# Performance work log

Measured on AMD Instinct MI355X. Metric: run time of the kernel, lower is better.

Reference implementation:

```python
import jax, jax.numpy as jnp
import numpy as np

H, W = 256, 256
N = 1024          # gaussians
G = 2             # num_gabor
RANK = 6          # abundance channels / endmembers
C = 128           # spectral bands
LORA_ALPHA = 0.1


def setup_inputs() -> dict:
    key = jax.random.key(0)
    ks = jax.random.split(key, 8)
    xyz = 0.5 * jax.random.normal(ks[0], (N, 2), jnp.float32)          # pre-tanh means
    cholesky = jnp.zeros((N, 3), jnp.float32)                           # + bound -> identity-ish cov
    feat0 = jnp.log(jnp.expm1(jnp.float32(0.05)))                       # inverse softplus(0.05)
    features_dc = feat0 + 0.01 * jax.random.normal(ks[1], (N, RANK), jnp.float32)
    gabor_freqs = (jax.random.uniform(ks[2], (N * G, 2), jnp.float32) - 0.5) * 0.002
    gabor_weights = jax.random.uniform(ks[3], (N * G, 1), jnp.float32) * -5.0
    lora_U = 0.3 * jax.random.normal(ks[4], (RANK, 2), jnp.float32)
    lora_V = 0.001 * jax.random.normal(ks[5], (2, C), jnp.float32)
    lora_scale_logit = jnp.zeros((1,), jnp.float32)
    opacity = jnp.ones((N, 1), jnp.float32)
    endmember = jax.random.uniform(ks[6], (RANK, C), jnp.float32)
    return {"xyz": xyz, "cholesky": cholesky, "features_dc": features_dc,
            "gabor_freqs": gabor_freqs, "gabor_weights": gabor_weights,
            "lora_U": lora_U, "lora_V": lora_V, "lora_scale_logit": lora_scale_logit,
            "opacity": opacity, "endmember": endmember}


def _rasterize_gabor_sum(xyz, cholesky, features_dc, gabor_freqs, gabor_weights, opacity):
    # project_gaussians_2d: tanh means in [-1,1] -> pixel coords
    means = jnp.tanh(xyz)                                               # [N,2]
    centers = (means * 0.5 + 0.5) * jnp.array([W, H], jnp.float32)      # [N,2] (x,y)
    ch = cholesky + jnp.array([0.5, 0.0, 0.5], jnp.float32)             # cholesky bound
    l1, l2, l3 = ch[:, 0], ch[:, 1], ch[:, 2]
    # Sigma = L L^T, L = [[l1,0],[l2,l3]] -> conic = Sigma^{-1}
    a = l1 * l1
    b = l1 * l2
    c = l2 * l2 + l3 * l3
    det = a * c - b * b
    ca, cb, cc = c / det, -b / det, a / det                             # [N]
    # pixel grid, row-major flat index p = y*W + x, pixel centers at +0.5
    xs = jnp.arange(W, dtype=jnp.float32) + 0.5
    ys = jnp.arange(H, dtype=jnp.float32) + 0.5
    px = jnp.tile(xs, H)                                                # [HW]
    py = jnp.repeat(ys, W)                                              # [HW]
    dx = px[None, :] - centers[:, 0:1]                                  # [N,HW]
    dy = py[None, :] - centers[:, 1:2]                                  # [N,HW]
    sigma = 0.5 * (ca[:, None] * dx * dx + cc[:, None] * dy * dy) + cb[:, None] * dx * dy
    gauss = jnp.where(sigma >= 0, jnp.exp(-sigma), 0.0)                 # [N,HW]
    # gabor modulation: 1 + sum_g w_g * cos(fx_g*dx + fy_g*dy)
    fx = jnp.exp(gabor_freqs[:, 0]).reshape(N, G)
    fy = jnp.exp(gabor_freqs[:, 1]).reshape(N, G)
    gw = jax.nn.sigmoid(gabor_weights[:, 0]).reshape(N, G)
    mod = jnp.ones_like(gauss)
    for g in range(G):  # small fixed loop over gabor components
        mod = mod + gw[:, g:g + 1] * jnp.cos(fx[:, g:g + 1] * dx + fy[:, g:g + 1] * dy)
    wmat = gauss * mod                                                  # [N,HW]
    feats = jax.nn.softplus(features_dc) * opacity                      # [N,RANK]
    # sum-blending rasterization (background = 0); linear in features so
    # the 3/4-channel group split in the original concatenates to the same result
    abundance = jnp.einsum('np,nr->pr', wmat, feats)                    # [HW,RANK]
    return jnp.maximum(abundance, 0.0)


def reference(xyz, cholesky, features_dc, gabor_freqs, gabor_weights,
              lora_U, lora_V, lora_scale_logit, opacity, endmember):
    abundance = _rasterize_gabor_sum(xyz, cholesky, features_dc,
                                     gabor_freqs, gabor_weights, opacity)
    # LoRA-calibrated endmember
    delta = jnp.tanh(lora_U @ lora_V)                                   # [RANK,C]
    scale = LORA_ALPHA * jnp.tanh(lora_scale_logit[0])
    E = jnp.clip(endmember + scale * delta, 1e-6, None)
    render = (abundance @ E).reshape(1, H, W, C).transpose(0, 3, 1, 2)  # [1,C,H,W]
    return render, abundance, E
```

## Files before the change

kernel.cpp:

```cpp
#include <hip/hip_runtime.h>
#include <math.h>

#define HH 256
#define WW 256
#define NPTS 1024
#define RANK 6
#define NC 128
#define PIX (HH * WW)
#define PSTRIDE 20
#define MAXG 160
#define SEG 128

typedef float vf4 __attribute__((ext_vector_type(4)));

__device__ __forceinline__ float softplus_f(float x) {
    return fmaxf(x, 0.0f) + log1pf(__expf(-fabsf(x)));
}

__global__ __launch_bounds__(256) void fused_kernel(
    const float* __restrict__ xyz, const float* __restrict__ chol,
    const float* __restrict__ fdc, const float* __restrict__ gfreq,
    const float* __restrict__ gwt, const float* __restrict__ opac,
    const float* __restrict__ lU, const float* __restrict__ lV,
    const float* __restrict__ lS, const float* __restrict__ em,
    float* __restrict__ render, float* __restrict__ abund,
    float* __restrict__ Eout)
{
    __shared__ float Els[NC * 8];
    __shared__ float glist[MAXG * PSTRIDE];
    __shared__ int   idxl[4 * SEG];
    __shared__ int   wcnt[4];
    __shared__ float accT[RANK * 4 * 64];
    __shared__ float accR[RANK * 64];

    const int t    = threadIdx.x;
    const int tile = blockIdx.x;
    const int tx   = (tile & 3) * 64;
    const int ty   = tile >> 2;
    const int wv   = t >> 6;
    const int ln   = t & 63;
    const float px = (float)(tx + ln) + 0.5f;
    const float py = (float)ty + 0.5f;

    {
        float scale = 0.1f * tanhf(lS[0]);
#pragma unroll
        for (int k = 0; k < 3; ++k) {
            int i = k * 256 + t;
            int r = i >> 7; int c = i & 127;
            float dot = lU[r * 2] * lV[c] + lU[r * 2 + 1] * lV[NC + c];
            float e = fmaxf(em[i] + scale * tanhf(dot), 1e-6f);
            Els[c * 8 + r] = e;
            if (tile == 0) Eout[i] = e;
        }
    }

    const float txmin = (float)tx, txmax = (float)(tx + 64);
    const float tymin = (float)ty, tymax = (float)(ty + 1);
    {
        int cnt = 0;
        const int gbase = wv * 256;
        for (int k = 0; k < 4; ++k) {
            const int gid = gbase + k * 64 + ln;
            float cx = (tanhf(xyz[gid * 2 + 0]) * 0.5f + 0.5f) * (float)WW;
            float cy = (tanhf(xyz[gid * 2 + 1]) * 0.5f + 0.5f) * (float)HH;
            float l1 = chol[gid * 3 + 0] + 0.5f;
            float l2 = chol[gid * 3 + 1];
            float l3 = chol[gid * 3 + 2] + 0.5f;
            float a = l1 * l1;
            float c = l2 * l2 + l3 * l3;
            float rx = 6.0f * sqrtf(a);
            float ry = 6.0f * sqrtf(c);
            bool hit = (cx - rx <= txmax) && (cx + rx >= txmin) &&
                       (cy - ry <= tymax) && (cy + ry >= tymin);
            unsigned long long m = __ballot(hit);
            if (hit) {
                int pos = cnt + __popcll(m & ((1ull << ln) - 1ull));
                if (pos < SEG) idxl[wv * SEG + pos] = gid;
            }
            cnt += __popcll(m);
        }
        if (ln == 0) wcnt[wv] = min(cnt, SEG);
    }
    __syncthreads();

    const int c0 = wcnt[0], c1 = wcnt[1], c2 = wcnt[2], c3 = wcnt[3];
    const int o1 = c0, o2 = c0 + c1, o3 = o2 + c2;
    int T = o3 + c3;
    if (T > MAXG) T = MAXG;

    for (int j = t; j < T; j += 256) {
        int w, o;
        if (j < o1)      { w = 0; o = j; }
        else if (j < o2) { w = 1; o = j - o1; }
        else if (j < o3) { w = 2; o = j - o2; }
        else             { w = 3; o = j - o3; }
        const int n = idxl[w * SEG + o];
        float cx = (tanhf(xyz[n * 2 + 0]) * 0.5f + 0.5f) * (float)WW;
        float cy = (tanhf(xyz[n * 2 + 1]) * 0.5f + 0.5f) * (float)HH;
        float l1 = chol[n * 3 + 0] + 0.5f;
        float l2 = chol[n * 3 + 1];
        float l3 = chol[n * 3 + 2] + 0.5f;
        float a = l1 * l1, bb = l1 * l2, c = l2 * l2 + l3 * l3;
        float inv = 1.0f / (a * c - bb * bb);
        float* g = glist + j * PSTRIDE;
        g[0] = cx; g[1] = cy;
        g[2] = c * inv; g[3] = -bb * inv; g[4] = a * inv;
        g[5] = __expf(gfreq[n * 4 + 0]);
        g[6] = __expf(gfreq[n * 4 + 1]);
        g[7] = __expf(gfreq[n * 4 + 2]);
        g[8] = __expf(gfreq[n * 4 + 3]);
        g[9]  = 1.0f / (1.0f + __expf(-gwt[n * 2 + 0]));
        g[10] = 1.0f / (1.0f + __expf(-gwt[n * 2 + 1]));
        float op = opac[n];
#pragma unroll
        for (int r = 0; r < RANK; ++r)
            g[11 + r] = softplus_f(fdc[n * RANK + r]) * op;
    }
    __syncthreads();

    float acc[RANK] = {0.f, 0.f, 0.f, 0.f, 0.f, 0.f};
    for (int i = wv; i < T; i += 4) {
        const vf4* gv = (const vf4*)(glist + i * PSTRIDE);
        vf4 g0 = gv[0];
        vf4 g1 = gv[1];
        vf4 g2 = gv[2];
        float dx = px - g0.x;
        float dy = py - g0.y;
        float sigma = 0.5f * (g0.z * dx * dx + g1.x * dy * dy) + g0.w * dx * dy;
        vf4 g3 = gv[3];
        vf4 g4 = gv[4];
        float wm = __expf(-sigma) *
                   (1.0f + g2.y * __cosf(g1.y * dx + g1.z * dy)
                         + g2.z * __cosf(g1.w * dx + g2.x * dy));
        wm = (sigma >= 0.0f) ? wm : 0.0f;
        acc[0] = fmaf(wm, g2.w, acc[0]);
        acc[1] = fmaf(wm, g3.x, acc[1]);
        acc[2] = fmaf(wm, g3.y, acc[2]);
        acc[3] = fmaf(wm, g3.z, acc[3]);
        acc[4] = fmaf(wm, g3.w, acc[4]);
        acc[5] = fmaf(wm, g4.x, acc[5]);
    }
#pragma unroll
    for (int r = 0; r < RANK; ++r)
        accT[r * 256 + t] = acc[r];
    __syncthreads();

    for (int v = t; v < RANK * 64; v += 256) {
        int r = v >> 6, u = v & 63;
        const float* row = accT + r * 256;
        float s = (row[u] + row[64 + u]) + (row[128 + u] + row[192 + u]);
        accR[v] = fmaxf(s, 0.0f);
    }
    __syncthreads();

    if (t < 96) {
        vf4 q;
#pragma unroll
        for (int k = 0; k < 4; ++k) {
            int v = t * 4 + k;
            int pl = v / 6;
            int r  = v - pl * 6;
            q[k] = accR[r * 64 + pl];
        }
        __builtin_nontemporal_store(
            q, (vf4*)(abund + (size_t)(ty * WW + tx) * RANK) + t);
    }

    const int pxo = (ln & 15) * 4;
    vf4 ab[RANK];
#pragma unroll
    for (int r = 0; r < RANK; ++r)
        ab[r] = *(const vf4*)(accR + r * 64 + pxo);

    float* rp = render + ty * WW + tx + pxo;
#pragma unroll
    for (int i = 0; i < 8; ++i) {
        const int cl = wv * 32 + i * 4 + (ln >> 4);
        const vf4 e0 = *(const vf4*)(Els + cl * 8);
        const vf4 e1 = *(const vf4*)(Els + cl * 8 + 4);
        vf4 o = ab[0] * e0.x;
        o += ab[1] * e0.y;
        o += ab[2] * e0.z;
        o += ab[3] * e0.w;
        o += ab[4] * e1.x;
        o += ab[5] * e1.y;
        __builtin_nontemporal_store(o, (vf4*)(rp + (size_t)cl * PIX));
    }
}

extern "C" void kernel_launch(void* const* d_in, const int* in_sizes, int n_in,
                              void* d_out, int out_size, void* d_ws, size_t ws_size,
                              hipStream_t stream)
{
    const float* xyz             = (const float*)d_in[0];
    const float* cholesky        = (const float*)d_in[1];
    const float* features_dc     = (const float*)d_in[2];
    const float* gabor_freqs     = (const float*)d_in[3];
    const float* gabor_weights   = (const float*)d_in[4];
    const float* lora_U          = (const float*)d_in[5];
    const float* lora_V          = (const float*)d_in[6];
    const float* lora_scale_logit= (const float*)d_in[7];
    const float* opacity         = (const float*)d_in[8];
    const float* endmember       = (const float*)d_in[9];

    float* out    = (float*)d_out;
    float* render = out;
    float* abund  = out + (size_t)NC * PIX;
    float* Eout   = abund + (size_t)PIX * RANK;

    fused_kernel<<<1024, 256, 0, stream>>>(
        xyz, cholesky, features_dc, gabor_freqs, gabor_weights, opacity,
        lora_U, lora_V, lora_scale_logit, endmember, render, abund, Eout);
}
```

Baseline: 17.69 us.

## Process one full image row per block with 512 threads

Each block now covers a full 256-pixel row instead of a 64-pixel quarter row, and the launch drops from 1024 blocks of 256 threads to 256 blocks of 512. Gaussian culling tests only the y extent and splits the gaussian list between two thread halves rather than four waves. The goal is to cut the per-block culling and parameter preprocessing that was repeated four times per row, and to write full contiguous rows to the outputs. Nontemporal stores are replaced by plain stores. Costs are fewer blocks (256 on a large GPU, so lower occupancy), more gaussians per block, and a higher MAXG cap.

```diff
diff --git a/kernel.cpp b/kernel.cpp
--- a/kernel.cpp
+++ b/kernel.cpp
@@ -8,8 +8,8 @@
 #define NC 128
 #define PIX (HH * WW)
 #define PSTRIDE 20
-#define MAXG 160
-#define SEG 128
+#define MAXG 256
+#define SEG 64
 
 typedef float vf4 __attribute__((ext_vector_type(4)));
 
@@ -17,7 +17,7 @@
     return fmaxf(x, 0.0f) + log1pf(__expf(-fabsf(x)));
 }
 
-__global__ __launch_bounds__(256) void fused_kernel(
+__global__ __launch_bounds__(512) void fused_kernel(
     const float* __restrict__ xyz, const float* __restrict__ chol,
     const float* __restrict__ fdc, const float* __restrict__ gfreq,
     const float* __restrict__ gwt, const float* __restrict__ opac,
@@ -28,51 +28,43 @@
 {
     __shared__ float Els[NC * 8];
     __shared__ float glist[MAXG * PSTRIDE];
-    __shared__ int   idxl[4 * SEG];
-    __shared__ int   wcnt[4];
-    __shared__ float accT[RANK * 4 * 64];
-    __shared__ float accR[RANK * 64];
-
-    const int t    = threadIdx.x;
-    const int tile = blockIdx.x;
-    const int tx   = (tile & 3) * 64;
-    const int ty   = tile >> 2;
-    const int wv   = t >> 6;
-    const int ln   = t & 63;
-    const float px = (float)(tx + ln) + 0.5f;
-    const float py = (float)ty + 0.5f;
+    __shared__ int   idxl[8 * SEG];
+    __shared__ int   wcnt[8];
+    __shared__ float accT[RANK * 512];
+    __shared__ float accR[RANK * 256];
+
+    const int t  = threadIdx.x;
+    const int y  = blockIdx.x;
+    const int wv = t >> 6;
+    const int ln = t & 63;
+    const int pxl = t & 255;
+    const int half = t >> 8;
+    const float px = (float)pxl + 0.5f;
+    const float py = (float)y + 0.5f;
 
     {
         float scale = 0.1f * tanhf(lS[0]);
-#pragma unroll
-        for (int k = 0; k < 3; ++k) {
-            int i = k * 256 + t;
+        for (int i = t; i < RANK * NC; i += 512) {
             int r = i >> 7; int c = i & 127;
             float dot = lU[r * 2] * lV[c] + lU[r * 2 + 1] * lV[NC + c];
             float e = fmaxf(em[i] + scale * tanhf(dot), 1e-6f);
             Els[c * 8 + r] = e;
-            if (tile == 0) Eout[i] = e;
+            if (y == 0) Eout[i] = e;
         }
     }
 
-    const float txmin = (float)tx, txmax = (float)(tx + 64);
-    const float tymin = (float)ty, tymax = (float)(ty + 1);
+    const float tymin = (float)y, tymax = (float)(y + 1);
     {
         int cnt = 0;
-        const int gbase = wv * 256;
-        for (int k = 0; k < 4; ++k) {
+        const int gbase = wv * 128;
+        for (int k = 0; k < 2; ++k) {
             const int gid = gbase + k * 64 + ln;
-            float cx = (tanhf(xyz[gid * 2 + 0]) * 0.5f + 0.5f) * (float)WW;
             float cy = (tanhf(xyz[gid * 2 + 1]) * 0.5f + 0.5f) * (float)HH;
-            float l1 = chol[gid * 3 + 0] + 0.5f;
             float l2 = chol[gid * 3 + 1];
             float l3 = chol[gid * 3 + 2] + 0.5f;
-            float a = l1 * l1;
             float c = l2 * l2 + l3 * l3;
-            float rx = 6.0f * sqrtf(a);
             float ry = 6.0f * sqrtf(c);
-            bool hit = (cx - rx <= txmax) && (cx + rx >= txmin) &&
-                       (cy - ry <= tymax) && (cy + ry >= tymin);
+            bool hit = (cy - ry <= tymax) && (cy + ry >= tymin);
             unsigned long long m = __ballot(hit);
             if (hit) {
                 int pos = cnt + __popcll(m & ((1ull << ln) - 1ull));
@@ -84,18 +76,20 @@
     }
     __syncthreads();
 
-    const int c0 = wcnt[0], c1 = wcnt[1], c2 = wcnt[2], c3 = wcnt[3];
-    const int o1 = c0, o2 = c0 + c1, o3 = o2 + c2;
-    int T = o3 + c3;
+    int off[8];
+    {
+        int s = 0;
+#pragma unroll
+        for (int w = 0; w < 8; ++w) { off[w] = s; s += wcnt[w]; }
+    }
+    int T = off[7] + wcnt[7];
     if (T > MAXG) T = MAXG;
 
-    for (int j = t; j < T; j += 256) {
-        int w, o;
-        if (j < o1)      { w = 0; o = j; }
-        else if (j < o2) { w = 1; o = j - o1; }
-        else if (j < o3) { w = 2; o = j - o2; }
-        else             { w = 3; o = j - o3; }
-        const int n = idxl[w * SEG + o];
+    for (int j = t; j < T; j += 512) {
+        int w = 0;
+#pragma unroll
+        for (int q = 1; q < 8; ++q) { if (j >= off[q]) w = q; }
+        const int n = idxl[w * SEG + (j - off[w])];
         float cx = (tanhf(xyz[n * 2 + 0]) * 0.5f + 0.5f) * (float)WW;
         float cy = (tanhf(xyz[n * 2 + 1]) * 0.5f + 0.5f) * (float)HH;
         float l1 = chol[n * 3 + 0] + 0.5f;
@@ -120,7 +114,7 @@
     __syncthreads();
 
     float acc[RANK] = {0.f, 0.f, 0.f, 0.f, 0.f, 0.f};
-    for (int i = wv; i < T; i += 4) {
+    for (int i = half; i < T; i += 2) {
         const vf4* gv = (const vf4*)(glist + i * PSTRIDE);
         vf4 g0 = gv[0];
         vf4 g1 = gv[1];
@@ -143,49 +137,46 @@
     }
 #pragma unroll
     for (int r = 0; r < RANK; ++r)
-        accT[r * 256 + t] = acc[r];
-    __syncthreads();
-
-    for (int v = t; v < RANK * 64; v += 256) {
-        int r = v >> 6, u = v & 63;
-        const float* row = accT + r * 256;
-        float s = (row[u] + row[64 + u]) + (row[128 + u] + row[192 + u]);
+        accT[r * 512 + t] = acc[r];
+    __syncthreads();
+
+    for (int v = t; v < RANK * 256; v += 512) {
+        int r = v >> 8, u = v & 255;
+        float s = accT[r * 512 + u] + accT[r * 512 + 256 + u];
         accR[v] = fmaxf(s, 0.0f);
     }
     __syncthreads();
 
-    if (t < 96) {
+    if (t < 384) {
         vf4 q;
 #pragma unroll
         for (int k = 0; k < 4; ++k) {
             int v = t * 4 + k;
             int pl = v / 6;
             int r  = v - pl * 6;
-            q[k] = accR[r * 64 + pl];
+            q[k] = accR[r * 256 + pl];
         }
-        __builtin_nontemporal_store(
-            q, (vf4*)(abund + (size_t)(ty * WW + tx) * RANK) + t);
-    }
-
-    const int pxo = (ln & 15) * 4;
+        *((vf4*)(abund + (size_t)y * WW * RANK) + t) = q;
+    }
+
     vf4 ab[RANK];
 #pragma unroll
     for (int r = 0; r < RANK; ++r)
-        ab[r] = *(const vf4*)(accR + r * 64 + pxo);
-
-    float* rp = render + ty * WW + tx + pxo;
-#pragma unroll
-    for (int i = 0; i < 8; ++i) {
-        const int cl = wv * 32 + i * 4 + (ln >> 4);
-        const vf4 e0 = *(const vf4*)(Els + cl * 8);
-        const vf4 e1 = *(const vf4*)(Els + cl * 8 + 4);
+        ab[r] = *(const vf4*)(accR + r * 256 + ln * 4);
+
+    float* rp = render + (size_t)y * WW + (size_t)ln * 4;
+#pragma unroll
+    for (int i = 0; i < 16; ++i) {
+        const int c = wv * 16 + i;
+        const vf4 e0 = *(const vf4*)(Els + c * 8);
+        const vf4 e1 = *(const vf4*)(Els + c * 8 + 4);
         vf4 o = ab[0] * e0.x;
         o += ab[1] * e0.y;
         o += ab[2] * e0.z;
         o += ab[3] * e0.w;
         o += ab[4] * e1.x;
         o += ab[5] * e1.y;
-        __builtin_nontemporal_store(o, (vf4*)(rp + (size_t)cl * PIX));
+        *((vf4*)(rp + (size_t)c * PIX)) = o;
     }
 }
 
@@ -209,7 +200,7 @@
     float* abund  = out + (size_t)NC * PIX;
     float* Eout   = abund + (size_t)PIX * RANK;
 
-    fused_kernel<<<1024, 256, 0, stream>>>(
+    fused_kernel<<<HH, 512, 0, stream>>>(
         xyz, cholesky, features_dc, gabor_freqs, gabor_weights, opacity,
         lora_U, lora_V, lora_scale_logit, endmember, render, abund, Eout);
 }
```

Result: slower. 20.34 us (+15.0%).
